# Optimization experiments

Measured on AMD Instinct MI355X. Metric: run time of the kernel, lower is better.

## Reference

```python
import jax, jax.numpy as jnp
import numpy as np

N_NODES = 50000
DROPOUT_P = 0.5


def _spmm(edge_src, edge_dst, edge_weight, h):
    # out[d] = sum_{e: dst[e]==d} w[e] * h[src[e]]  -- sparse Laplacian aggregation
    msgs = edge_weight[:, None] * h[edge_src]          # [E, F]
    return jax.ops.segment_sum(msgs, edge_dst, num_segments=N_NODES)


def setup_inputs() -> dict:
    key = jax.random.key(0)
    ks = jax.random.split(key, 8)
    E = 1600000
    nfeat, nhid, nclass = 512, 256, 40
    return {
        "x": jax.random.normal(ks[0], (N_NODES, nfeat), dtype=jnp.float32),
        "edge_src": jax.random.randint(ks[1], (E,), 0, N_NODES, dtype=jnp.int32),
        "edge_dst": jax.random.randint(ks[2], (E,), 0, N_NODES, dtype=jnp.int32),
        "edge_weight": jax.random.normal(ks[3], (E,), dtype=jnp.float32) * 0.05,
        "W1": jax.random.normal(ks[4], (nfeat, nhid), dtype=jnp.float32) * 0.05,
        "b1": jax.random.normal(ks[5], (nhid,), dtype=jnp.float32) * 0.05,
        "W2": jax.random.normal(ks[6], (nhid, nclass), dtype=jnp.float32) * 0.05,
        "b2": jax.random.normal(ks[7], (nclass,), dtype=jnp.float32) * 0.05,
    }


def reference(x, edge_src, edge_dst, edge_weight, W1, b1, W2, b2):
    # layer 1: dense GEMM -> sparse aggregate -> bias -> ReLU -> dropout
    h = x @ W1
    h = _spmm(edge_src, edge_dst, edge_weight, h)
    h = jax.nn.relu(h + b1)
    # dropout with a fixed key (deterministic, matches train-mode scaling 1/(1-p))
    keep = jax.random.bernoulli(jax.random.key(42), 1.0 - DROPOUT_P, h.shape)
    h = jnp.where(keep, h / (1.0 - DROPOUT_P), 0.0)
    # layer 2: dense GEMM -> sparse aggregate -> bias
    o = h @ W2
    o = _spmm(edge_src, edge_dst, edge_weight, o)
    return o + b2
```

## Files before the change

### kernel.cpp

```cpp
#include <hip/hip_runtime.h>

typedef short bf16x8 __attribute__((ext_vector_type(8)));
typedef float f32x4 __attribute__((ext_vector_type(4)));

constexpr int N_NODES = 50000;
constexpr int F_IN    = 512;
constexpr int F_HID   = 256;
constexpr int F_OUT   = 40;
constexpr int SCAN_BLOCKS = (N_NODES + 255) / 256;

__device__ __forceinline__ float bf2f(unsigned short u) {
  return __uint_as_float(((unsigned)u) << 16);
}
__device__ __forceinline__ unsigned short f2bf(float f) {
  unsigned x = __float_as_uint(f);
  x += 0x7FFFu + ((x >> 16) & 1u);
  return (unsigned short)(x >> 16);
}

__device__ __forceinline__ bf16x8 cvt8(f32x4 a, f32x4 b) {
  bf16x8 o;
  o[0] = (short)f2bf(a[0]); o[1] = (short)f2bf(a[1]);
  o[2] = (short)f2bf(a[2]); o[3] = (short)f2bf(a[3]);
  o[4] = (short)f2bf(b[0]); o[5] = (short)f2bf(b[1]);
  o[6] = (short)f2bf(b[2]); o[7] = (short)f2bf(b[3]);
  return o;
}

__device__ __forceinline__ unsigned tf_rotl(unsigned x, int d) {
  return (x << d) | (x >> (32 - d));
}
__device__ __forceinline__ unsigned threefry_bits(unsigned i) {
  const unsigned k0 = 0u, k1 = 42u, k2 = 0x1BD11BDAu ^ 0u ^ 42u;
  unsigned x0 = 0u + k0, x1 = i + k1;
#define TF_R(r) { x0 += x1; x1 = tf_rotl(x1, (r)) ^ x0; }
  TF_R(13) TF_R(15) TF_R(26) TF_R(6)   x0 += k1; x1 += k2 + 1u;
  TF_R(17) TF_R(29) TF_R(16) TF_R(24)  x0 += k2; x1 += k0 + 2u;
  TF_R(13) TF_R(15) TF_R(26) TF_R(6)   x0 += k0; x1 += k1 + 3u;
  TF_R(17) TF_R(29) TF_R(16) TF_R(24)  x0 += k1; x1 += k2 + 4u;
  TF_R(13) TF_R(15) TF_R(26) TF_R(6)   x0 += k2; x1 += k0 + 5u;
#undef TF_R
  return x0 ^ x1;
}

__global__ void k_zero(int* __restrict__ p, int n) {
  int i = blockIdx.x * 256 + threadIdx.x;
  if (i < n) p[i] = 0;
}

__global__ void k_hist(const int* __restrict__ dst, int* __restrict__ deg, int E) {
  int e = blockIdx.x * 256 + threadIdx.x;
  if (e < E) atomicAdd(&deg[dst[e]], 1);
}

__global__ __launch_bounds__(256) void k_scan_part(const int* __restrict__ deg,
                                                   int* __restrict__ bsum) {
  __shared__ int red[256];
  int t = threadIdx.x;
  int i = blockIdx.x * 256 + t;
  red[t] = (i < N_NODES) ? deg[i] : 0;
  __syncthreads();
#pragma unroll
  for (int off = 128; off > 0; off >>= 1) {
    if (t < off) red[t] += red[t + off];
    __syncthreads();
  }
  if (t == 0) bsum[blockIdx.x] = red[0];
}

__global__ __launch_bounds__(256) void k_scan_base(int* __restrict__ bsum,
                                                   int* __restrict__ offs) {
  __shared__ int sh[256];
  int t = threadIdx.x;
  int v = (t < SCAN_BLOCKS) ? bsum[t] : 0;
  sh[t] = v;
  __syncthreads();
#pragma unroll
  for (int off = 1; off < 256; off <<= 1) {
    int x = (t >= off) ? sh[t - off] : 0;
    __syncthreads();
    sh[t] += x;
    __syncthreads();
  }
  if (t < SCAN_BLOCKS) bsum[t] = sh[t] - v;
  if (t == 255) offs[N_NODES] = sh[255];
}

__global__ __launch_bounds__(256) void k_scan_final(int* __restrict__ deg,
                                                    const int* __restrict__ bsum,
                                                    int* __restrict__ offs) {
  __shared__ int sh[256];
  int t = threadIdx.x;
  int i = blockIdx.x * 256 + t;
  int v = (i < N_NODES) ? deg[i] : 0;
  sh[t] = v;
  __syncthreads();
#pragma unroll
  for (int off = 1; off < 256; off <<= 1) {
    int x = (t >= off) ? sh[t - off] : 0;
    __syncthreads();
    sh[t] += x;
    __syncthreads();
  }
  if (i < N_NODES) {
    offs[i] = bsum[blockIdx.x] + sh[t] - v;
    deg[i] = 0;
  }
}

__global__ void k_scatter(const int* __restrict__ src, const int* __restrict__ dst,
                          const float* __restrict__ w,
                          const int* __restrict__ offs, int* __restrict__ cursor,
                          unsigned* __restrict__ ep, int E) {
  int e = blockIdx.x * 256 + threadIdx.x;
  if (e < E) {
    int d = dst[e];
    int pos = offs[d] + atomicAdd(&cursor[d], 1);
    if (pos >= 0 && pos < E)
      ep[pos] = ((unsigned)src[e] << 16) | (unsigned)f2bf(w[e]);
  }
}

__global__ void k_wt(const float* __restrict__ W1, unsigned short* __restrict__ wT) {
  int i = blockIdx.x * 256 + threadIdx.x;
  if (i < F_IN * F_HID) {
    int c = i >> 9, k = i & 511;
    wT[i] = f2bf(W1[(size_t)k * F_HID + c]);
  }
}

__global__ __launch_bounds__(256) void k_gemm1m(const float* __restrict__ X,
                                                const unsigned short* __restrict__ wT,
                                                unsigned short* __restrict__ h1h,
                                                int half) {
  int t = threadIdx.x;
  int wave = t >> 6, lane = t & 63, q = lane >> 4, r = lane & 15;
  int r0 = blockIdx.x * 64;
  int arow = r0 + wave * 16 + r;
  if (arow > N_NODES - 1) arow = N_NODES - 1;
  const float* xrow = X + (size_t)arow * F_IN + q * 8;
  const unsigned short* bl = wT + (size_t)half * 128 * F_IN + (size_t)r * F_IN + q * 8;
  f32x4 acc[8];
#pragma unroll
  for (int n = 0; n < 8; ++n) acc[n] = (f32x4){0.f, 0.f, 0.f, 0.f};

#pragma unroll 2
  for (int k0 = 0; k0 < F_IN; k0 += 64) {
    f32x4 a0 = *(const f32x4*)(xrow + k0);
    f32x4 a1 = *(const f32x4*)(xrow + k0 + 4);
    f32x4 a2 = *(const f32x4*)(xrow + k0 + 32);
    f32x4 a3 = *(const f32x4*)(xrow + k0 + 32 + 4);
    bf16x8 A0 = cvt8(a0, a1);
    bf16x8 A1 = cvt8(a2, a3);
#pragma unroll
    for (int n = 0; n < 8; ++n) {
      bf16x8 b0 = *(const bf16x8*)(bl + (size_t)n * 16 * F_IN + k0);
      acc[n] = __builtin_amdgcn_mfma_f32_16x16x32_bf16(A0, b0, acc[n], 0, 0, 0);
    }
#pragma unroll
    for (int n = 0; n < 8; ++n) {
      bf16x8 b1 = *(const bf16x8*)(bl + (size_t)n * 16 * F_IN + k0 + 32);
      acc[n] = __builtin_amdgcn_mfma_f32_16x16x32_bf16(A1, b1, acc[n], 0, 0, 0);
    }
  }
  int mrow = r0 + wave * 16 + q * 4;
#pragma unroll
  for (int n = 0; n < 8; ++n) {
#pragma unroll
    for (int tt = 0; tt < 4; ++tt) {
      int row = mrow + tt;
      if (row < N_NODES) h1h[(size_t)row * 128 + n * 16 + r] = f2bf(acc[n][tt]);
    }
  }
}

__global__ __launch_bounds__(256) void k_agg1h(const ushort2* __restrict__ h1h2,
                                               const int* __restrict__ offs,
                                               const unsigned* __restrict__ ep,
                                               const float* __restrict__ b1,
                                               const float* __restrict__ W2,
                                               float* __restrict__ o1, int half) {
  __shared__ unsigned short w2h[128 * F_OUT];
  __shared__ float hrow[4][128];
  int t = threadIdx.x;
  for (int i = t; i < 128 * F_OUT; i += 256) {
    int k = i / F_OUT, j = i - k * F_OUT;
    w2h[i] = f2bf(W2[(size_t)(half * 128 + k) * F_OUT + j]);
  }
  int wave = t >> 6, lane = t & 63;
  int wid = blockIdx.x * 4 + wave;
  int s0 = offs[wid], s1 = offs[wid + 1];
  float a0 = 0.f, a1 = 0.f;
  int e = s0;
  for (; e + 4 <= s1; e += 4) {
    unsigned p0 = ep[e], p1 = ep[e + 1], p2 = ep[e + 2], p3 = ep[e + 3];
    ushort2 v0 = h1h2[(size_t)(p0 >> 16) * 64 + lane];
    ushort2 v1 = h1h2[(size_t)(p1 >> 16) * 64 + lane];
    ushort2 v2 = h1h2[(size_t)(p2 >> 16) * 64 + lane];
    ushort2 v3 = h1h2[(size_t)(p3 >> 16) * 64 + lane];
    float w0 = bf2f((unsigned short)p0), w1 = bf2f((unsigned short)p1);
    float w2 = bf2f((unsigned short)p2), w3 = bf2f((unsigned short)p3);
    a0 = fmaf(w0, bf2f(v0.x), a0); a1 = fmaf(w0, bf2f(v0.y), a1);
    a0 = fmaf(w1, bf2f(v1.x), a0); a1 = fmaf(w1, bf2f(v1.y), a1);
    a0 = fmaf(w2, bf2f(v2.x), a0); a1 = fmaf(w2, bf2f(v2.y), a1);
    a0 = fmaf(w3, bf2f(v3.x), a0); a1 = fmaf(w3, bf2f(v3.y), a1);
  }
  for (; e < s1; ++e) {
    unsigned pe = ep[e];
    float w = bf2f((unsigned short)pe);
    ushort2 v = h1h2[(size_t)(pe >> 16) * 64 + lane];
    a0 = fmaf(w, bf2f(v.x), a0);
    a1 = fmaf(w, bf2f(v.y), a1);
  }
  int c0 = lane * 2;
  int gc = half * 128 + c0;
  float r0 = fmaxf(a0 + b1[gc + 0], 0.f);
  float r1 = fmaxf(a1 + b1[gc + 1], 0.f);
  unsigned base = (unsigned)wid * 256u + (unsigned)gc;
  r0 = (threefry_bits(base + 0u) >> 31) ? 0.f : r0 * 2.f;
  r1 = (threefry_bits(base + 1u) >> 31) ? 0.f : r1 * 2.f;
  hrow[wave][c0 + 0] = r0;
  hrow[wave][c0 + 1] = r1;
  __syncthreads();
  if (lane < F_OUT) {
    float acc = 0.f;
#pragma unroll 8
    for (int k = 0; k < 128; ++k)
      acc = fmaf(hrow[wave][k], bf2f(w2h[k * F_OUT + lane]), acc);
    o1[(size_t)wid * F_OUT + lane] += acc;
  }
}

__global__ __launch_bounds__(256) void k_agg2(const float* __restrict__ o1,
                                              const int* __restrict__ offs,
                                              const unsigned* __restrict__ ep,
                                              const float* __restrict__ b2,
                                              float* __restrict__ out) {
  int wid  = (blockIdx.x << 2) + (threadIdx.x >> 6);
  int lane = threadIdx.x & 63;
  if (lane >= F_OUT) return;
  int s0 = offs[wid], s1 = offs[wid + 1];
  float acc = 0.f;
  int e = s0;
  for (; e + 4 <= s1; e += 4) {
    unsigned p0 = ep[e], p1 = ep[e + 1], p2 = ep[e + 2], p3 = ep[e + 3];
    float g0 = o1[(size_t)(p0 >> 16) * F_OUT + lane];
    float g1 = o1[(size_t)(p1 >> 16) * F_OUT + lane];
    float g2 = o1[(size_t)(p2 >> 16) * F_OUT + lane];
    float g3 = o1[(size_t)(p3 >> 16) * F_OUT + lane];
    acc = fmaf(bf2f((unsigned short)p0), g0, acc);
    acc = fmaf(bf2f((unsigned short)p1), g1, acc);
    acc = fmaf(bf2f((unsigned short)p2), g2, acc);
    acc = fmaf(bf2f((unsigned short)p3), g3, acc);
  }
  for (; e < s1; ++e) {
    unsigned pe = ep[e];
    acc = fmaf(bf2f((unsigned short)pe), o1[(size_t)(pe >> 16) * F_OUT + lane], acc);
  }
  out[(size_t)wid * F_OUT + lane] = acc + b2[lane];
}

extern "C" void kernel_launch(void* const* d_in, const int* in_sizes, int n_in,
                              void* d_out, int out_size, void* d_ws, size_t ws_size,
                              hipStream_t stream) {
  const float* x    = (const float*)d_in[0];
  const int*   esrc = (const int*)d_in[1];
  const int*   edst = (const int*)d_in[2];
  const float* ew   = (const float*)d_in[3];
  const float* W1   = (const float*)d_in[4];
  const float* b1   = (const float*)d_in[5];
  const float* W2   = (const float*)d_in[6];
  const float* b2   = (const float*)d_in[7];
  const int E = in_sizes[1];

  char* p = (char*)d_ws;
  auto alloc = [&](size_t bytes) { char* r = p; p += (bytes + 255) & ~(size_t)255; return r; };
  unsigned short* h1h  = (unsigned short*)alloc((size_t)N_NODES * 128 * 2);
  float*          o1   = (float*)alloc((size_t)N_NODES * F_OUT * 4);
  unsigned*       ep   = (unsigned*)alloc((size_t)E * 4);
  unsigned short* wT   = (unsigned short*)alloc((size_t)F_IN * F_HID * 2);
  int*            offs = (int*)alloc((size_t)(N_NODES + 1) * 4);
  int*            deg  = (int*)alloc((size_t)N_NODES * 4);
  int*            bsum = (int*)alloc((size_t)SCAN_BLOCKS * 4);

  int eb = (E + 255) / 256;
  k_zero<<<(N_NODES + 255) / 256, 256, 0, stream>>>(deg, N_NODES);
  k_zero<<<(N_NODES * F_OUT + 255) / 256, 256, 0, stream>>>((int*)o1, N_NODES * F_OUT);
  k_wt<<<(F_IN * F_HID + 255) / 256, 256, 0, stream>>>(W1, wT);
  k_hist<<<eb, 256, 0, stream>>>(edst, deg, E);
  k_scan_part<<<SCAN_BLOCKS, 256, 0, stream>>>(deg, bsum);
  k_scan_base<<<1, 256, 0, stream>>>(bsum, offs);
  k_scan_final<<<SCAN_BLOCKS, 256, 0, stream>>>(deg, bsum, offs);
  k_scatter<<<eb, 256, 0, stream>>>(esrc, edst, ew, offs, deg, ep, E);

  int gblocks = (N_NODES + 63) / 64;
  for (int half = 0; half < 2; ++half) {
    k_gemm1m<<<gblocks, 256, 0, stream>>>(x, wT, h1h, half);
    k_agg1h<<<N_NODES / 4, 256, 0, stream>>>((const ushort2*)h1h, offs, ep, b1, W2, o1, half);
  }
  k_agg2<<<N_NODES / 4, 256, 0, stream>>>(o1, offs, ep, b2, (float*)d_out);
}
```

Before: 700.8 us.

## Prefetch GEMM B fragments, vectorize edge loads, transpose W2 in LDS

The GEMM1 kernel now double-buffers its W1 fragments in registers and fully unrolls the K loop, so B loads overlap the MFMAs. Both aggregation kernels align the edge cursor to a multiple of 4 and then read packed edges as uint4, unrolling 8 edges per iteration to keep more gathers in flight. In agg1, W2 is stored transposed and padded in LDS so each lane reads contiguous ushort4 and float4 vectors in the small 128x40 product. The risks are higher register pressure from the unrolling and the buffers, and more branches for the alignment prologue and epilogue.

```diff
diff --git a/kernel.cpp b/kernel.cpp
--- a/kernel.cpp
+++ b/kernel.cpp
@@ -144,24 +144,33 @@
 #pragma unroll
   for (int n = 0; n < 8; ++n) acc[n] = (f32x4){0.f, 0.f, 0.f, 0.f};
 
-#pragma unroll 2
+  bf16x8 BA[8], BB[8];
+#pragma unroll
+  for (int n = 0; n < 8; ++n)
+    BA[n] = *(const bf16x8*)(bl + (size_t)n * 16 * F_IN);
+
+#pragma unroll
   for (int k0 = 0; k0 < F_IN; k0 += 64) {
     f32x4 a0 = *(const f32x4*)(xrow + k0);
     f32x4 a1 = *(const f32x4*)(xrow + k0 + 4);
     f32x4 a2 = *(const f32x4*)(xrow + k0 + 32);
-    f32x4 a3 = *(const f32x4*)(xrow + k0 + 32 + 4);
+    f32x4 a3 = *(const f32x4*)(xrow + k0 + 36);
     bf16x8 A0 = cvt8(a0, a1);
     bf16x8 A1 = cvt8(a2, a3);
 #pragma unroll
-    for (int n = 0; n < 8; ++n) {
-      bf16x8 b0 = *(const bf16x8*)(bl + (size_t)n * 16 * F_IN + k0);
-      acc[n] = __builtin_amdgcn_mfma_f32_16x16x32_bf16(A0, b0, acc[n], 0, 0, 0);
+    for (int n = 0; n < 8; ++n)
+      BB[n] = *(const bf16x8*)(bl + (size_t)n * 16 * F_IN + k0 + 32);
+#pragma unroll
+    for (int n = 0; n < 8; ++n)
+      acc[n] = __builtin_amdgcn_mfma_f32_16x16x32_bf16(A0, BA[n], acc[n], 0, 0, 0);
+    if (k0 + 64 < F_IN) {
+#pragma unroll
+      for (int n = 0; n < 8; ++n)
+        BA[n] = *(const bf16x8*)(bl + (size_t)n * 16 * F_IN + k0 + 64);
     }
 #pragma unroll
-    for (int n = 0; n < 8; ++n) {
-      bf16x8 b1 = *(const bf16x8*)(bl + (size_t)n * 16 * F_IN + k0 + 32);
-      acc[n] = __builtin_amdgcn_mfma_f32_16x16x32_bf16(A1, b1, acc[n], 0, 0, 0);
-    }
+    for (int n = 0; n < 8; ++n)
+      acc[n] = __builtin_amdgcn_mfma_f32_16x16x32_bf16(A1, BB[n], acc[n], 0, 0, 0);
   }
   int mrow = r0 + wave * 16 + q * 4;
 #pragma unroll
@@ -180,38 +189,67 @@
                                                const float* __restrict__ b1,
                                                const float* __restrict__ W2,
                                                float* __restrict__ o1, int half) {
-  __shared__ unsigned short w2h[128 * F_OUT];
+  __shared__ unsigned short w2t[F_OUT * 132];
   __shared__ float hrow[4][128];
   int t = threadIdx.x;
-  for (int i = t; i < 128 * F_OUT; i += 256) {
-    int k = i / F_OUT, j = i - k * F_OUT;
-    w2h[i] = f2bf(W2[(size_t)(half * 128 + k) * F_OUT + j]);
+  for (int i = t; i < F_OUT * 128; i += 256) {
+    int j = i >> 7, k = i & 127;
+    w2t[j * 132 + k] = f2bf(W2[(size_t)(half * 128 + k) * F_OUT + j]);
   }
   int wave = t >> 6, lane = t & 63;
   int wid = blockIdx.x * 4 + wave;
   int s0 = offs[wid], s1 = offs[wid + 1];
   float a0 = 0.f, a1 = 0.f;
+
+#define AGG1_EDGE(P) {                                        \
+    float w_ = bf2f((unsigned short)(P));                     \
+    ushort2 v_ = h1h2[(size_t)((P) >> 16) * 64 + lane];       \
+    a0 = fmaf(w_, bf2f(v_.x), a0);                            \
+    a1 = fmaf(w_, bf2f(v_.y), a1); }
+
   int e = s0;
-  for (; e + 4 <= s1; e += 4) {
-    unsigned p0 = ep[e], p1 = ep[e + 1], p2 = ep[e + 2], p3 = ep[e + 3];
-    ushort2 v0 = h1h2[(size_t)(p0 >> 16) * 64 + lane];
-    ushort2 v1 = h1h2[(size_t)(p1 >> 16) * 64 + lane];
-    ushort2 v2 = h1h2[(size_t)(p2 >> 16) * 64 + lane];
-    ushort2 v3 = h1h2[(size_t)(p3 >> 16) * 64 + lane];
-    float w0 = bf2f((unsigned short)p0), w1 = bf2f((unsigned short)p1);
-    float w2 = bf2f((unsigned short)p2), w3 = bf2f((unsigned short)p3);
+  while (e < s1 && (e & 3)) { AGG1_EDGE(ep[e]); ++e; }
+  for (; e + 8 <= s1; e += 8) {
+    uint4 qa = *(const uint4*)(ep + e);
+    uint4 qb = *(const uint4*)(ep + e + 4);
+    ushort2 v0 = h1h2[(size_t)(qa.x >> 16) * 64 + lane];
+    ushort2 v1 = h1h2[(size_t)(qa.y >> 16) * 64 + lane];
+    ushort2 v2 = h1h2[(size_t)(qa.z >> 16) * 64 + lane];
+    ushort2 v3 = h1h2[(size_t)(qa.w >> 16) * 64 + lane];
+    ushort2 v4 = h1h2[(size_t)(qb.x >> 16) * 64 + lane];
+    ushort2 v5 = h1h2[(size_t)(qb.y >> 16) * 64 + lane];
+    ushort2 v6 = h1h2[(size_t)(qb.z >> 16) * 64 + lane];
+    ushort2 v7 = h1h2[(size_t)(qb.w >> 16) * 64 + lane];
+    float w0 = bf2f((unsigned short)qa.x), w1 = bf2f((unsigned short)qa.y);
+    float w2 = bf2f((unsigned short)qa.z), w3 = bf2f((unsigned short)qa.w);
+    float w4 = bf2f((unsigned short)qb.x), w5 = bf2f((unsigned short)qb.y);
+    float w6 = bf2f((unsigned short)qb.z), w7 = bf2f((unsigned short)qb.w);
     a0 = fmaf(w0, bf2f(v0.x), a0); a1 = fmaf(w0, bf2f(v0.y), a1);
     a0 = fmaf(w1, bf2f(v1.x), a0); a1 = fmaf(w1, bf2f(v1.y), a1);
     a0 = fmaf(w2, bf2f(v2.x), a0); a1 = fmaf(w2, bf2f(v2.y), a1);
     a0 = fmaf(w3, bf2f(v3.x), a0); a1 = fmaf(w3, bf2f(v3.y), a1);
-  }
-  for (; e < s1; ++e) {
-    unsigned pe = ep[e];
-    float w = bf2f((unsigned short)pe);
-    ushort2 v = h1h2[(size_t)(pe >> 16) * 64 + lane];
-    a0 = fmaf(w, bf2f(v.x), a0);
-    a1 = fmaf(w, bf2f(v.y), a1);
-  }
+    a0 = fmaf(w4, bf2f(v4.x), a0); a1 = fmaf(w4, bf2f(v4.y), a1);
+    a0 = fmaf(w5, bf2f(v5.x), a0); a1 = fmaf(w5, bf2f(v5.y), a1);
+    a0 = fmaf(w6, bf2f(v6.x), a0); a1 = fmaf(w6, bf2f(v6.y), a1);
+    a0 = fmaf(w7, bf2f(v7.x), a0); a1 = fmaf(w7, bf2f(v7.y), a1);
+  }
+  if (e + 4 <= s1) {
+    uint4 qa = *(const uint4*)(ep + e);
+    ushort2 v0 = h1h2[(size_t)(qa.x >> 16) * 64 + lane];
+    ushort2 v1 = h1h2[(size_t)(qa.y >> 16) * 64 + lane];
+    ushort2 v2 = h1h2[(size_t)(qa.z >> 16) * 64 + lane];
+    ushort2 v3 = h1h2[(size_t)(qa.w >> 16) * 64 + lane];
+    float w0 = bf2f((unsigned short)qa.x), w1 = bf2f((unsigned short)qa.y);
+    float w2 = bf2f((unsigned short)qa.z), w3 = bf2f((unsigned short)qa.w);
+    a0 = fmaf(w0, bf2f(v0.x), a0); a1 = fmaf(w0, bf2f(v0.y), a1);
+    a0 = fmaf(w1, bf2f(v1.x), a0); a1 = fmaf(w1, bf2f(v1.y), a1);
+    a0 = fmaf(w2, bf2f(v2.x), a0); a1 = fmaf(w2, bf2f(v2.y), a1);
+    a0 = fmaf(w3, bf2f(v3.x), a0); a1 = fmaf(w3, bf2f(v3.y), a1);
+    e += 4;
+  }
+  for (; e < s1; ++e) AGG1_EDGE(ep[e]);
+#undef AGG1_EDGE
+
   int c0 = lane * 2;
   int gc = half * 128 + c0;
   float r0 = fmaxf(a0 + b1[gc + 0], 0.f);
@@ -223,10 +261,18 @@
   hrow[wave][c0 + 1] = r1;
   __syncthreads();
   if (lane < F_OUT) {
+    const unsigned short* wrow = &w2t[lane * 132];
+    const float* hr = hrow[wave];
     float acc = 0.f;
-#pragma unroll 8
-    for (int k = 0; k < 128; ++k)
-      acc = fmaf(hrow[wave][k], bf2f(w2h[k * F_OUT + lane]), acc);
+#pragma unroll
+    for (int k0 = 0; k0 < 128; k0 += 4) {
+      ushort4 wv = *(const ushort4*)(wrow + k0);
+      float4  hv = *(const float4*)(hr + k0);
+      acc = fmaf(hv.x, bf2f(wv.x), acc);
+      acc = fmaf(hv.y, bf2f(wv.y), acc);
+      acc = fmaf(hv.z, bf2f(wv.z), acc);
+      acc = fmaf(hv.w, bf2f(wv.w), acc);
+    }
     o1[(size_t)wid * F_OUT + lane] += acc;
   }
 }
@@ -241,22 +287,47 @@
   if (lane >= F_OUT) return;
   int s0 = offs[wid], s1 = offs[wid + 1];
   float acc = 0.f;
+
+#define AGG2_EDGE(P) \
+    acc = fmaf(bf2f((unsigned short)(P)), o1[(size_t)((P) >> 16) * F_OUT + lane], acc);
+
   int e = s0;
-  for (; e + 4 <= s1; e += 4) {
-    unsigned p0 = ep[e], p1 = ep[e + 1], p2 = ep[e + 2], p3 = ep[e + 3];
-    float g0 = o1[(size_t)(p0 >> 16) * F_OUT + lane];
-    float g1 = o1[(size_t)(p1 >> 16) * F_OUT + lane];
-    float g2 = o1[(size_t)(p2 >> 16) * F_OUT + lane];
-    float g3 = o1[(size_t)(p3 >> 16) * F_OUT + lane];
-    acc = fmaf(bf2f((unsigned short)p0), g0, acc);
-    acc = fmaf(bf2f((unsigned short)p1), g1, acc);
-    acc = fmaf(bf2f((unsigned short)p2), g2, acc);
-    acc = fmaf(bf2f((unsigned short)p3), g3, acc);
-  }
-  for (; e < s1; ++e) {
-    unsigned pe = ep[e];
-    acc = fmaf(bf2f((unsigned short)pe), o1[(size_t)(pe >> 16) * F_OUT + lane], acc);
-  }
+  while (e < s1 && (e & 3)) { AGG2_EDGE(ep[e]); ++e; }
+  for (; e + 8 <= s1; e += 8) {
+    uint4 qa = *(const uint4*)(ep + e);
+    uint4 qb = *(const uint4*)(ep + e + 4);
+    float g0 = o1[(size_t)(qa.x >> 16) * F_OUT + lane];
+    float g1 = o1[(size_t)(qa.y >> 16) * F_OUT + lane];
+    float g2 = o1[(size_t)(qa.z >> 16) * F_OUT + lane];
+    float g3 = o1[(size_t)(qa.w >> 16) * F_OUT + lane];
+    float g4 = o1[(size_t)(qb.x >> 16) * F_OUT + lane];
+    float g5 = o1[(size_t)(qb.y >> 16) * F_OUT + lane];
+    float g6 = o1[(size_t)(qb.z >> 16) * F_OUT + lane];
+    float g7 = o1[(size_t)(qb.w >> 16) * F_OUT + lane];
+    acc = fmaf(bf2f((unsigned short)qa.x), g0, acc);
+    acc = fmaf(bf2f((unsigned short)qa.y), g1, acc);
+    acc = fmaf(bf2f((unsigned short)qa.z), g2, acc);
+    acc = fmaf(bf2f((unsigned short)qa.w), g3, acc);
+    acc = fmaf(bf2f((unsigned short)qb.x), g4, acc);
+    acc = fmaf(bf2f((unsigned short)qb.y), g5, acc);
+    acc = fmaf(bf2f((unsigned short)qb.z), g6, acc);
+    acc = fmaf(bf2f((unsigned short)qb.w), g7, acc);
+  }
+  if (e + 4 <= s1) {
+    uint4 qa = *(const uint4*)(ep + e);
+    float g0 = o1[(size_t)(qa.x >> 16) * F_OUT + lane];
+    float g1 = o1[(size_t)(qa.y >> 16) * F_OUT + lane];
+    float g2 = o1[(size_t)(qa.z >> 16) * F_OUT + lane];
+    float g3 = o1[(size_t)(qa.w >> 16) * F_OUT + lane];
+    acc = fmaf(bf2f((unsigned short)qa.x), g0, acc);
+    acc = fmaf(bf2f((unsigned short)qa.y), g1, acc);
+    acc = fmaf(bf2f((unsigned short)qa.z), g2, acc);
+    acc = fmaf(bf2f((unsigned short)qa.w), g3, acc);
+    e += 4;
+  }
+  for (; e < s1; ++e) AGG2_EDGE(ep[e]);
+#undef AGG2_EDGE
+
   out[(size_t)wid * F_OUT + lane] = acc + b2[lane];
 }
 
```

Result: slower. 818.0 us (+16.7%).
